# Optimization experiments

Hardware: AMD Instinct MI355X
Metric: run time of the kernel (lower is better)

The kernel has to match this reference:

```python
import jax, jax.numpy as jnp
import numpy as np

NEG = -10000.0


def _build_label_vocab():
    vocab = {'O': 0}
    i = 1
    for t in ['PER', 'ORG', 'LOC', 'MISC']:
        for p in ['B', 'I', 'E', 'S']:
            vocab[f'{p}-{t}'] = i
            i += 1
    return vocab


def _init_transition(key):
    """Random transition with BIOES constraints, matching CRF.initialize()."""
    vocab = _build_label_vocab()
    L = len(vocab) + 2          # 19 (17 labels + start + end)
    start, end = L - 2, L - 1
    T = np.array(jax.random.normal(key, (L, L)), dtype=np.float32)
    T[:, end] = NEG
    T[start, :] = NEG
    for lf, i_f in vocab.items():
        pf, tf = ('O', 'O') if lf == 'O' else lf.split('-')
        for lt, i_t in vocab.items():
            pt, tt = ('O', 'O') if lt == 'O' else lt.split('-')
            allowed = (pf in ('O', 'E', 'S') and pt in ('O', 'B', 'S')) or \
                      (pf in ('B', 'I') and pt in ('I', 'E') and tf == tt)
            if not allowed:
                T[i_t, i_f] = NEG
    return jnp.asarray(T)


def setup_inputs() -> dict:
    key = jax.random.key(0)
    k1, k2, k3, k4 = jax.random.split(key, 4)
    B, S, NL = 4096, 256, 17
    logits = jax.random.normal(k1, (B, S, NL), dtype=jnp.float32)
    labels = jax.random.randint(k2, (B, S), 0, NL)
    lens = jax.random.randint(k3, (B,), 1, S + 1)   # lengths in [1, S]
    transition = _init_transition(k4)                # [19, 19]
    return {"logits": logits, "labels": labels, "lens": lens,
            "transition": transition}


def reference(logits, labels, lens, transition):
    """CRF log-likelihood: gold_score(pad_logits(logits)) - norm_score."""
    B, S, NL = logits.shape
    L = transition.shape[0]       # label_size = NL + 2
    start, end = L - 2, L - 1

    # pad_logits: append start/end columns with -10000
    pads = jnp.full((B, S, 2), NEG, dtype=logits.dtype)
    logits_p = jnp.concatenate([logits, pads], axis=2)   # [B, S, L]

    tmask = (jnp.arange(S)[None, :] < lens[:, None])     # [B, S] valid tokens

    # ---- gold score ----
    # unary: gather emission score of the gold label at each position
    unary = jnp.take_along_axis(logits_p, labels[:, :, None], axis=2)[:, :, 0]
    unary = (unary * tmask.astype(logits.dtype)).sum(axis=1)

    # binary: transition scores along the gold path (with start/end padding)
    labels_ext = jnp.concatenate(
        [jnp.full((B, 1), start, labels.dtype), labels,
         jnp.full((B, 1), end, labels.dtype)], axis=1)   # [B, S+2]
    emask = jnp.arange(S + 2)[None, :] < (lens + 1)[:, None]
    labels_ext = jnp.where(emask, labels_ext, end)
    trn_scr = transition[labels_ext[:, 1:], labels_ext[:, :-1]]  # [B, S+1]
    bmask = (jnp.arange(S + 1)[None, :] < (lens + 1)[:, None]).astype(logits.dtype)
    binary = (trn_scr * bmask).sum(axis=1)

    gold = unary + binary

    # ---- partition (norm) score: forward algorithm over time ----
    alpha0 = jnp.full((B, L), NEG, dtype=logits.dtype).at[:, start].set(0.0)

    def step(alpha, xs):
        logit, m = xs  # logit: [B, L], m: [B] bool (position < len)
        # alpha_nxt[b,i] = logit[b,i] + LSE_j(alpha[b,j] + T[i,j])
        nxt = logit + jax.nn.logsumexp(alpha[:, None, :] + transition[None], axis=2)
        alpha = jnp.where(m[:, None], nxt, alpha)
        return alpha, None

    alpha, _ = jax.lax.scan(step, alpha0,
                            (jnp.swapaxes(logits_p, 0, 1), tmask.T))
    alpha = alpha + transition[end][None, :]
    norm = jax.nn.logsumexp(alpha, axis=1)

    return gold - norm   # [B] per-sequence log-likelihood
```

## Files before the change

### kernel.cpp

```cpp
#include <hip/hip_runtime.h>

constexpr int S   = 256;
constexpr int NL  = 17;
constexpr int L   = 19;
constexpr int WPB = 2;

__global__ __launch_bounds__(64 * WPB)
void crf_fwd(const float* __restrict__ logits,
             const int*   __restrict__ labels,
             const int*   __restrict__ lens,
             const float* __restrict__ transition,
             float* __restrict__ out, int totalElemM1)
{
    __shared__ float Tsh[L * L];
    __shared__ __align__(16) float pbuf[WPB][2][2][32];

    const int tid  = threadIdx.x;
    const int wave = tid >> 6;
    const int wtid = tid & 63;
    const int half = wtid >> 5;
    const int lane = wtid & 31;
    const int b    = blockIdx.x * WPB + wave;

    for (int k = tid; k < L * L; k += 64 * WPB) Tsh[k] = transition[k];
    __syncthreads();

    const int  i    = lane;
    const bool act  = (i < L);
    const bool emit = (i < NL);
    const int  ic   = act ? i : 0;

    float coef[L];
    #pragma unroll
    for (int j = 0; j < L; ++j)
        coef[j] = __expf(half ? Tsh[j * L + ic] : Tsh[ic * L + j]);

    const int len = lens[b];
    const int mid = len >> 1;
    const int nb  = len - 1 - mid;
    const int nup = half ? nb : mid;
    const int nsteps = (mid + 7) & ~7;

    const int seqbase = b * (S * NL);

    float p = act ? __expf(half ? Tsh[(L - 1) * L + ic]
                                : Tsh[ic * L + (L - 2)])
                  : 0.0f;
    float m = 0.0f;

    const char* lgbase = (const char*)logits;
    const int capHiF = 4 * min(seqbase + (S - 1) * NL + i, totalElemM1);
    const int capHi  = half ? 0x7ffffffc : capHiF;
    const int capLo  = half ? 4 * (seqbase + i) : 0;
    const int stride = half ? -(8 * NL * 4) : (8 * NL * 4);

    int   off[8];
    float lgbuf[8];
    #pragma unroll
    for (int u = 0; u < 8; ++u) {
        int tok = half ? (len - 1 - u) : u;
        tok = tok > 0 ? tok : 0;
        int o = 4 * (seqbase + tok * NL + i);
        o = min(o, capHiF);
        off[u] = o;
        lgbuf[u] = *(const float*)(lgbase + o);
    }

    for (int tb = 0; tb < nsteps; tb += 8) {
        #pragma unroll
        for (int u = 0; u < 8; ++u) {
            const int   t  = tb + u;
            const float lg = lgbuf[u];
            int o = off[u] + stride;
            o = max(o, capLo);
            o = min(o, capHi);
            off[u] = o;
            lgbuf[u] = *(const float*)(lgbase + o);

            const bool upd = (t < nup);

            const float el = emit ? __expf(lg) : 0.0f;
            const float pe = p * el;

            float* pb = &pbuf[wave][half][u & 1][0];
            pb[i] = pe;
            asm volatile("" ::: "memory");
            const float4* q = (const float4*)pb;
            const float4 q0 = q[0], q1 = q[1], q2 = q[2], q3 = q[3], q4 = q[4];

            float a0 = q0.x * coef[0];
            float a1 = q0.y * coef[1];
            float a2 = q0.z * coef[2];
            float a3 = q0.w * coef[3];
            a0 = fmaf(q1.x, coef[4],  a0);
            a1 = fmaf(q1.y, coef[5],  a1);
            a2 = fmaf(q1.z, coef[6],  a2);
            a3 = fmaf(q1.w, coef[7],  a3);
            a0 = fmaf(q2.x, coef[8],  a0);
            a1 = fmaf(q2.y, coef[9],  a1);
            a2 = fmaf(q2.z, coef[10], a2);
            a3 = fmaf(q2.w, coef[11], a3);
            a0 = fmaf(q3.x, coef[12], a0);
            a1 = fmaf(q3.y, coef[13], a1);
            a2 = fmaf(q3.z, coef[14], a2);
            a3 = fmaf(q3.w, coef[15], a3);
            a0 = fmaf(q4.x, coef[16], a0);
            a1 = fmaf(q4.y, coef[17], a1);
            a2 = fmaf(q4.z, coef[18], a2);

            float pn = (a0 + a1) + (a2 + a3);

            if ((u & 3) == 3) {
                float m0 = fmaxf(fmaxf(q0.x, q0.y), fmaxf(q0.z, q0.w));
                float m1 = fmaxf(fmaxf(q1.x, q1.y), fmaxf(q1.z, q1.w));
                float m2 = fmaxf(fmaxf(q2.x, q2.y), fmaxf(q2.z, q2.w));
                float m3 = fmaxf(fmaxf(q3.x, q3.y), fmaxf(q3.z, q3.w));
                float m4 = fmaxf(fmaxf(q4.x, q4.y), q4.z);
                float mx = fmaxf(fmaxf(m0, m1), fmaxf(fmaxf(m2, m3), m4));
                pn *= __frcp_rn(mx);
                m += upd ? __logf(mx) : 0.0f;
            }
            p = upd ? pn : p;
        }
    }

    {
        float lgf = 0.0f;
        if (half && emit) lgf = logits[(size_t)(seqbase + mid * NL + i)];
        if (half) p = emit ? p * __expf(lgf) : 0.0f;
    }

    const float other = __shfl_xor(p, 32);
    float prod = act ? p * other : 0.0f;
    #pragma unroll
    for (int o = 16; o >= 1; o >>= 1) prod += __shfl_xor(prod, o, 32);
    const float mtot = m + __shfl_xor(m, 32);
    const float norm = mtot + __logf(prod);

    const int* labp = labels + b * S;
    float gsum = 0.0f;
    for (int c = 0; c < len; c += 64) {
        const int tok = c + wtid;
        if (tok < len) {
            const int lab = labp[tok];
            const int prv = (tok == 0) ? (L - 2) : labp[tok - 1];
            gsum += logits[(size_t)(seqbase + tok * NL + lab)] + Tsh[lab * L + prv];
        }
    }
    #pragma unroll
    for (int o = 32; o >= 1; o >>= 1) gsum += __shfl_xor(gsum, o);
    const float gold = gsum + Tsh[(L - 1) * L + labp[len - 1]];

    if (wtid == 0) out[b] = gold - norm;
}

extern "C" void kernel_launch(void* const* d_in, const int* in_sizes, int n_in,
                              void* d_out, int out_size, void* d_ws, size_t ws_size,
                              hipStream_t stream)
{
    (void)n_in; (void)out_size; (void)d_ws; (void)ws_size;
    const float* logits     = (const float*)d_in[0];
    const int*   labels     = (const int*)d_in[1];
    const int*   lens       = (const int*)d_in[2];
    const float* transition = (const float*)d_in[3];
    float*       out        = (float*)d_out;
    const int B = in_sizes[2];
    const int totalElemM1 = B * S * NL - 1;
    crf_fwd<<<dim3(B / WPB), dim3(64 * WPB), 0, stream>>>(
        logits, labels, lens, transition, out, totalElemM1);
}
```

Before: 136.2 us.

## Exploit BIOES transition sparsity and schedule sequences longest-first

Replaces the dense 19-wide matvec per step with a sparsity-aware one. Allowed-transition groups are encoded in a constant signature table: 'heavy' lanes do a 9-term dot product, while 'light' lanes only combine a pair of shared entries. The running max is computed once by a designated lane and broadcast through shared memory. A one-block counting-sort kernel orders sequences by descending length so that long sequences launch first, and launches change to one wave per block. The aim is fewer FMAs and LDS reads per step plus better tail load balancing, at the cost of an extra kernel launch and a dependence on the BIOES structure of the transition matrix.

```diff
diff --git a/kernel.cpp b/kernel.cpp
--- a/kernel.cpp
+++ b/kernel.cpp
@@ -1,57 +1,103 @@
 #include <hip/hip_runtime.h>
 
-constexpr int S   = 256;
-constexpr int NL  = 17;
-constexpr int L   = 19;
-constexpr int WPB = 2;
-
-__global__ __launch_bounds__(64 * WPB)
+constexpr int S  = 256;
+constexpr int NL = 17;
+constexpr int L  = 19;
+
+__constant__ int c_sig[2][18] = {
+  {0, 3,4, 7,8, 11,12, 15,16,  0, 1,2, 5,6, 9,10, 13,14},
+  {0, 1,4, 5,8, 9,12, 13,16,   0, 2,3, 6,7, 10,11, 14,15},
+};
+
+__global__ __launch_bounds__(256)
+void sched_kernel(const int* __restrict__ lens, int* __restrict__ perm, int B)
+{
+    __shared__ int hist[256];
+    __shared__ int scanbuf[256];
+    const int t = threadIdx.x;
+    hist[t] = 0;
+    __syncthreads();
+    for (int s = t; s < B; s += 256) atomicAdd(&hist[256 - lens[s]], 1);
+    __syncthreads();
+    const int v = hist[t];
+    scanbuf[t] = v;
+    __syncthreads();
+    for (int d = 1; d < 256; d <<= 1) {
+        const int add = (t >= d) ? scanbuf[t - d] : 0;
+        __syncthreads();
+        scanbuf[t] += add;
+        __syncthreads();
+    }
+    hist[t] = scanbuf[t] - v;
+    __syncthreads();
+    for (int s = t; s < B; s += 256) {
+        const int pos = atomicAdd(&hist[256 - lens[s]], 1);
+        perm[pos] = s;
+    }
+}
+
+__global__ __launch_bounds__(64)
 void crf_fwd(const float* __restrict__ logits,
              const int*   __restrict__ labels,
              const int*   __restrict__ lens,
              const float* __restrict__ transition,
+             const int*   __restrict__ perm,
              float* __restrict__ out, int totalElemM1)
 {
     __shared__ float Tsh[L * L];
-    __shared__ __align__(16) float pbuf[WPB][2][2][32];
+    __shared__ __align__(16) float pbuf[2][2][32];
+    __shared__ float ebuf[2][20];
 
     const int tid  = threadIdx.x;
-    const int wave = tid >> 6;
-    const int wtid = tid & 63;
-    const int half = wtid >> 5;
-    const int lane = wtid & 31;
-    const int b    = blockIdx.x * WPB + wave;
-
-    for (int k = tid; k < L * L; k += 64 * WPB) Tsh[k] = transition[k];
-    __syncthreads();
-
-    const int  i    = lane;
-    const bool act  = (i < L);
-    const bool emit = (i < NL);
-    const int  ic   = act ? i : 0;
-
-    float coef[L];
-    #pragma unroll
-    for (int j = 0; j < L; ++j)
-        coef[j] = __expf(half ? Tsh[j * L + ic] : Tsh[ic * L + j]);
+    const int half = tid >> 5;
+    const int slot = tid & 31;
+    const int b    = perm ? perm[blockIdx.x] : (int)blockIdx.x;
+
+    for (int k = tid; k < L * L; k += 64) Tsh[k] = transition[k];
+    if (slot == 9) { pbuf[half][0][9] = 1.0f; pbuf[half][1][9] = 1.0f; }
+    __syncthreads();
+
+    const bool emit  = (slot < 18) && (slot != 9);
+    const int  d     = emit ? c_sig[half][slot] : 0;
+    const bool heavy = emit && ((slot < 9) ? ((slot & 1) == 0)
+                                           : ((slot & 1) == (half ? 1 : 0)));
+    const bool hvx   = heavy || (slot == 9);
+    const bool light = emit && !heavy;
+
+    float ch[9];
+    #pragma unroll
+    for (int j = 0; j < 9; ++j) {
+        const int s = c_sig[half][j];
+        ch[j] = heavy ? __expf(half ? Tsh[s * L + d] : Tsh[d * L + s]) : 0.0f;
+    }
+    int kty = 0;
+    if (light) kty = (slot < 9) ? ((slot - 1) >> 1) : ((slot - 10 - (half ? 0 : 1)) >> 1);
+    const int pairSlot = 10 + 2 * kty;
+    float cl0 = 0.0f, cl1 = 0.0f;
+    if (light) {
+        const int s0 = c_sig[half][pairSlot], s1 = c_sig[half][pairSlot + 1];
+        cl0 = __expf(half ? Tsh[s0 * L + d] : Tsh[d * L + s0]);
+        cl1 = __expf(half ? Tsh[s1 * L + d] : Tsh[d * L + s1]);
+    }
 
     const int len = lens[b];
-    const int mid = len >> 1;
-    const int nb  = len - 1 - mid;
-    const int nup = half ? nb : mid;
-    const int nsteps = (mid + 7) & ~7;
+    const int mid = (len + 1) >> 1;
+    const int nf  = mid - 1;
+    const int nb  = len >> 1;
+    const int nup = half ? nb : nf;
+    const int nsteps = (nb + 7) & ~7;
 
     const int seqbase = b * (S * NL);
 
-    float p = act ? __expf(half ? Tsh[(L - 1) * L + ic]
-                                : Tsh[ic * L + (L - 2)])
-                  : 0.0f;
+    float p = emit ? __expf(half ? Tsh[(L - 1) * L + d]
+                                 : Tsh[d * L + (L - 2)])
+                   : 0.0f;
     float m = 0.0f;
 
     const char* lgbase = (const char*)logits;
-    const int capHiF = 4 * min(seqbase + (S - 1) * NL + i, totalElemM1);
+    const int capHiF = 4 * min(seqbase + (S - 1) * NL + d, totalElemM1);
     const int capHi  = half ? 0x7ffffffc : capHiF;
-    const int capLo  = half ? 4 * (seqbase + i) : 0;
+    const int capLo  = half ? 4 * seqbase : 0;
     const int stride = half ? -(8 * NL * 4) : (8 * NL * 4);
 
     int   off[8];
@@ -60,7 +106,7 @@
     for (int u = 0; u < 8; ++u) {
         int tok = half ? (len - 1 - u) : u;
         tok = tok > 0 ? tok : 0;
-        int o = 4 * (seqbase + tok * NL + i);
+        int o = 4 * (seqbase + tok * NL + d);
         o = min(o, capHiF);
         off[u] = o;
         lgbuf[u] = *(const float*)(lgbase + o);
@@ -78,66 +124,66 @@
             lgbuf[u] = *(const float*)(lgbase + o);
 
             const bool upd = (t < nup);
-
             const float el = emit ? __expf(lg) : 0.0f;
             const float pe = p * el;
 
-            float* pb = &pbuf[wave][half][u & 1][0];
-            pb[i] = pe;
+            float* pb = &pbuf[half][u & 1][0];
+            if (emit) pb[slot] = pe;
             asm volatile("" ::: "memory");
-            const float4* q = (const float4*)pb;
-            const float4 q0 = q[0], q1 = q[1], q2 = q[2], q3 = q[3], q4 = q[4];
-
-            float a0 = q0.x * coef[0];
-            float a1 = q0.y * coef[1];
-            float a2 = q0.z * coef[2];
-            float a3 = q0.w * coef[3];
-            a0 = fmaf(q1.x, coef[4],  a0);
-            a1 = fmaf(q1.y, coef[5],  a1);
-            a2 = fmaf(q1.z, coef[6],  a2);
-            a3 = fmaf(q1.w, coef[7],  a3);
-            a0 = fmaf(q2.x, coef[8],  a0);
-            a1 = fmaf(q2.y, coef[9],  a1);
-            a2 = fmaf(q2.z, coef[10], a2);
-            a3 = fmaf(q2.w, coef[11], a3);
-            a0 = fmaf(q3.x, coef[12], a0);
-            a1 = fmaf(q3.y, coef[13], a1);
-            a2 = fmaf(q3.z, coef[14], a2);
-            a3 = fmaf(q3.w, coef[15], a3);
-            a0 = fmaf(q4.x, coef[16], a0);
-            a1 = fmaf(q4.y, coef[17], a1);
-            a2 = fmaf(q4.z, coef[18], a2);
-
-            float pn = (a0 + a1) + (a2 + a3);
-
+
+            float v = 0.0f, mxv = 1.0f;
+            if (hvx) {
+                const float4 q0 = *(const float4*)(pb);
+                const float4 q1 = *(const float4*)(pb + 4);
+                const float2 q2 = *(const float2*)(pb + 8);
+                float a0 = q0.x * ch[0];
+                float a1 = q0.y * ch[1];
+                float a2 = q0.z * ch[2];
+                a0 = fmaf(q0.w, ch[3], a0);
+                a1 = fmaf(q1.x, ch[4], a1);
+                a2 = fmaf(q1.y, ch[5], a2);
+                a0 = fmaf(q1.z, ch[6], a0);
+                a1 = fmaf(q1.w, ch[7], a1);
+                a2 = fmaf(q2.x, ch[8], a2);
+                v = (a0 + a1) + a2;
+                mxv = q2.y;
+                if ((u & 3) == 2 && slot == 9) {
+                    float m0 = fmaxf(fmaxf(q0.x, q0.y), fmaxf(q0.z, q0.w));
+                    float m1 = fmaxf(fmaxf(q1.x, q1.y), fmaxf(q1.z, q1.w));
+                    pbuf[half][1][9] = fmaxf(fmaxf(m0, m1), q2.x);
+                }
+            } else {
+                const float2 pr = *(const float2*)(pb + pairSlot);
+                v = pr.x * cl0;
+                v = fmaf(pr.y, cl1, v);
+                if ((u & 3) == 3) mxv = pb[9];
+            }
+
+            float pn = v;
             if ((u & 3) == 3) {
-                float m0 = fmaxf(fmaxf(q0.x, q0.y), fmaxf(q0.z, q0.w));
-                float m1 = fmaxf(fmaxf(q1.x, q1.y), fmaxf(q1.z, q1.w));
-                float m2 = fmaxf(fmaxf(q2.x, q2.y), fmaxf(q2.z, q2.w));
-                float m3 = fmaxf(fmaxf(q3.x, q3.y), fmaxf(q3.z, q3.w));
-                float m4 = fmaxf(fmaxf(q4.x, q4.y), q4.z);
-                float mx = fmaxf(fmaxf(m0, m1), fmaxf(fmaxf(m2, m3), m4));
-                pn *= __frcp_rn(mx);
-                m += upd ? __logf(mx) : 0.0f;
+                pn *= __frcp_rn(mxv);
+                m += upd ? __logf(mxv) : 0.0f;
             }
             p = upd ? pn : p;
         }
     }
 
-    {
-        float lgf = 0.0f;
-        if (half && emit) lgf = logits[(size_t)(seqbase + mid * NL + i)];
-        if (half) p = emit ? p * __expf(lgf) : 0.0f;
-    }
-
-    const float other = __shfl_xor(p, 32);
-    float prod = act ? p * other : 0.0f;
-    #pragma unroll
-    for (int o = 16; o >= 1; o >>= 1) prod += __shfl_xor(prod, o, 32);
+    if (!half && emit) {
+        const float lgf = logits[(size_t)(seqbase + (mid - 1) * NL + d)];
+        p *= __expf(lgf);
+    }
+
+    if (emit) ebuf[half][d] = p;
+    asm volatile("" ::: "memory");
+    float prod = 0.0f;
+    if (slot < NL) prod = ebuf[0][slot] * ebuf[1][slot];
+    #pragma unroll
+    for (int o2 = 16; o2 >= 1; o2 >>= 1) prod += __shfl_xor(prod, o2, 32);
     const float mtot = m + __shfl_xor(m, 32);
     const float norm = mtot + __logf(prod);
 
     const int* labp = labels + b * S;
+    const int  wtid = tid;
     float gsum = 0.0f;
     for (int c = 0; c < len; c += 64) {
         const int tok = c + wtid;
@@ -148,7 +194,7 @@
         }
     }
     #pragma unroll
-    for (int o = 32; o >= 1; o >>= 1) gsum += __shfl_xor(gsum, o);
+    for (int o2 = 32; o2 >= 1; o2 >>= 1) gsum += __shfl_xor(gsum, o2);
     const float gold = gsum + Tsh[(L - 1) * L + labp[len - 1]];
 
     if (wtid == 0) out[b] = gold - norm;
@@ -158,7 +204,7 @@
                               void* d_out, int out_size, void* d_ws, size_t ws_size,
                               hipStream_t stream)
 {
-    (void)n_in; (void)out_size; (void)d_ws; (void)ws_size;
+    (void)n_in; (void)out_size;
     const float* logits     = (const float*)d_in[0];
     const int*   labels     = (const int*)d_in[1];
     const int*   lens       = (const int*)d_in[2];
@@ -166,6 +212,12 @@
     float*       out        = (float*)d_out;
     const int B = in_sizes[2];
     const int totalElemM1 = B * S * NL - 1;
-    crf_fwd<<<dim3(B / WPB), dim3(64 * WPB), 0, stream>>>(
-        logits, labels, lens, transition, out, totalElemM1);
+
+    int* perm = nullptr;
+    if (ws_size >= (size_t)B * sizeof(int)) {
+        perm = (int*)d_ws;
+        sched_kernel<<<dim3(1), dim3(256), 0, stream>>>(lens, perm, B);
+    }
+    crf_fwd<<<dim3(B), dim3(64), 0, stream>>>(
+        logits, labels, lens, transition, perm, out, totalElemM1);
 }
```

After: 136.8 us. No clear change (+0.4%).
